# Optimization experiments

Hardware: AMD Instinct MI355X
Metric: run time of the kernel (lower is better)

Reference implementation:

```python
import jax, jax.numpy as jnp
import numpy as np

N_NODES = 50000
N_EDGES = 1600000
IN_DIM, HID_DIM, OUT_DIM = 128, 128, 64


def setup_inputs() -> dict:
    key = jax.random.key(0)
    ks = jax.random.split(key, 6)
    x = jax.random.normal(ks[0], (N_NODES, IN_DIM), dtype=jnp.float32)
    W1 = jax.random.normal(ks[1], (IN_DIM, HID_DIM), dtype=jnp.float32) * (1.0 / np.sqrt(IN_DIM))
    b1 = jnp.zeros((HID_DIM,), dtype=jnp.float32)
    W2 = jax.random.normal(ks[2], (HID_DIM, OUT_DIM), dtype=jnp.float32) * (1.0 / np.sqrt(HID_DIM))
    b2 = jnp.zeros((OUT_DIM,), dtype=jnp.float32)
    src = jax.random.randint(ks[3], (N_EDGES,), 0, N_NODES, dtype=jnp.int32)
    dst = jax.random.randint(ks[4], (N_EDGES,), 0, N_NODES, dtype=jnp.int32)
    return {"x": x, "W1": W1, "b1": b1, "W2": W2, "b2": b2,
            "src": src, "dst": dst, "n_nodes": N_NODES}


def _degree_norms(src, dst, n_nodes):
    ones = jnp.ones(src.shape, dtype=jnp.float32)
    out_deg = jax.ops.segment_sum(ones, src, num_segments=n_nodes)
    in_deg = jax.ops.segment_sum(ones, dst, num_segments=n_nodes)
    # DGL clamps degrees to min 1 before taking -0.5 power
    out_norm = jnp.power(jnp.maximum(out_deg, 1.0), -0.5)
    in_norm = jnp.power(jnp.maximum(in_deg, 1.0), -0.5)
    return out_norm, in_norm


def _graph_conv(x, W, b, src, dst, out_norm, in_norm, n_nodes):
    # norm='both': scale src feats, project (W first: in>=out), aggregate, scale dst
    h = x * out_norm[:, None]
    h = h @ W                                   # [N, out_feats]
    agg = jax.ops.segment_sum(h[src], dst, num_segments=n_nodes)
    return agg * in_norm[:, None] + b


def reference(x, W1, b1, W2, b2, src, dst, n_nodes):
    out_norm, in_norm = _degree_norms(src, dst, n_nodes)
    h = _graph_conv(x, W1, b1, src, dst, out_norm, in_norm, n_nodes)
    h = jax.nn.relu(h)
    # F.dropout(training=self.training): identity in eval mode
    h = _graph_conv(h, W2, b2, src, dst, out_norm, in_norm, n_nodes)
    return h
```

## Files before the change

### kernel.cpp

```cpp
#include <hip/hip_runtime.h>
#include <cstdint>

#define N_NODES 50000
#define N_EDGES 1600000
#define NPAD 50048
#define NTILES (NPAD / 64)
#define DUMMY 50000

#define NCOARSE 196
#define CBLK 256
#define ECHUNK (N_EDGES / CBLK)

#define OSL2 2
#define ONPS2 (N_NODES / OSL2)
#define ONW (ONPS2 / 2)
#define OPARTS2 256
#define OCH2 (N_EDGES / OPARTS2)

typedef __attribute__((ext_vector_type(8))) _Float16 f16x8;
typedef __attribute__((ext_vector_type(2))) _Float16 f16x2;
typedef __attribute__((ext_vector_type(4))) float f32x4;

__device__ __forceinline__ unsigned f16rn(float f) {
    _Float16 h = (_Float16)f;
    return (unsigned)__builtin_bit_cast(unsigned short, h);
}
__device__ __forceinline__ f16x2 u2h(unsigned u) { return __builtin_bit_cast(f16x2, u); }
__device__ __forceinline__ f16x2 pk_xor_add(f16x2 s, int d) {
    unsigned u = __builtin_bit_cast(unsigned, s);
    unsigned o = (unsigned)__shfl_xor((int)u, d);
    return s + __builtin_bit_cast(f16x2, o);
}

__global__ void k_fuse1(const int* __restrict__ src, const int* __restrict__ dst,
                        const float* __restrict__ W1, const float* __restrict__ W2,
                        unsigned* __restrict__ counts, unsigned* __restrict__ partial,
                        unsigned* __restrict__ Wt1, unsigned* __restrict__ Wt2) {
    __shared__ unsigned sm[ONW];
    int b = blockIdx.x, tid = threadIdx.x;
    if (b < 512) {
        int slice = b & 1, part = b >> 1;
        int lo = slice * ONPS2;
        for (int i = tid; i < ONW; i += 256) sm[i] = 0;
        __syncthreads();
        int ebase = part * OCH2;
        for (int i = tid; i < OCH2; i += 256) {
            int sv = src[ebase + i] - lo;
            if ((unsigned)sv < (unsigned)ONPS2)
                atomicAdd(&sm[sv >> 1], 1u << ((sv & 1) * 16));
        }
        __syncthreads();
        unsigned* outp = partial + ((size_t)slice * OPARTS2 + part) * ONW;
        for (int i = tid; i < ONW; i += 256) outp[i] = sm[i];
    } else if (b < 768) {
        int b2 = b - 512;
        for (int i = tid; i < NCOARSE; i += 256) sm[i] = 0;
        __syncthreads();
        int base = b2 * ECHUNK;
        for (int i = tid; i < ECHUNK; i += 256)
            atomicAdd(&sm[(unsigned)dst[base + i] >> 8], 1u);
        __syncthreads();
        for (int i = tid; i < NCOARSE; i += 256)
            counts[b2 * NCOARSE + i] = sm[i];
    } else {
        int t = (b - 768) * 256 + tid;
        if (t < 128 * 64) {
            int n = t >> 6, kp = t & 63;
            Wt1[t] = f16rn(W1[(2 * kp) * 128 + n]) | (f16rn(W1[(2 * kp + 1) * 128 + n]) << 16);
        }
        if (t < 64 * 64) {
            int n = t >> 6, kp = t & 63;
            Wt2[t] = f16rn(W2[(2 * kp) * 64 + n]) | (f16rn(W2[(2 * kp + 1) * 64 + n]) << 16);
        }
    }
}

__global__ void k_scanA(const unsigned* __restrict__ counts, unsigned* __restrict__ woff,
                        unsigned* __restrict__ tot) {
    __shared__ unsigned s[256];
    int c = blockIdx.x, t = threadIdx.x;
    unsigned v = counts[t * NCOARSE + c];
    s[t] = v; __syncthreads();
    for (int o = 1; o < 256; o <<= 1) {
        unsigned u = (t >= o) ? s[t - o] : 0u;
        __syncthreads(); s[t] += u; __syncthreads();
    }
    woff[t * NCOARSE + c] = s[t] - v;
    if (t == 255) tot[c] = s[255];
}

__global__ void k_scanB(const unsigned* __restrict__ tot, unsigned* __restrict__ base,
                        unsigned* __restrict__ row_ptr) {
    __shared__ unsigned s[256];
    int t = threadIdx.x;
    unsigned v = (t < NCOARSE) ? tot[t] : 0u;
    s[t] = v; __syncthreads();
    for (int o = 1; o < 256; o <<= 1) {
        unsigned u = (t >= o) ? s[t - o] : 0u;
        __syncthreads(); s[t] += u; __syncthreads();
    }
    if (t < NCOARSE) base[t] = s[t] - v;
    if (t == NCOARSE - 1) base[NCOARSE] = s[t];
    if (t == 0) row_ptr[N_NODES] = N_EDGES;
}

__global__ void k_fuse2(const int* __restrict__ src, const int* __restrict__ dst,
                        const unsigned* __restrict__ base, const unsigned* __restrict__ woff,
                        int* __restrict__ tmp_s, int* __restrict__ tmp_d,
                        const unsigned* __restrict__ partial, float* __restrict__ on) {
    __shared__ unsigned cur[NCOARSE];
    int b = blockIdx.x, t = threadIdx.x;
    if (b < 256) {
        for (int i = t; i < NCOARSE; i += 256) cur[i] = base[i] + woff[b * NCOARSE + i];
        __syncthreads();
        int ebase = b * ECHUNK;
        for (int i = t; i < ECHUNK; i += 256) {
            int d = dst[ebase + i], sv = src[ebase + i];
            unsigned p = atomicAdd(&cur[(unsigned)d >> 8], 1u);
            tmp_d[p] = d; tmp_s[p] = sv;
        }
    } else {
        int tt = (b - 256) * 256 + t;
        if (tt < OSL2 * ONW) {
            int slice = tt / ONW, word = tt % ONW;
            const unsigned* p = partial + (size_t)slice * OPARTS2 * ONW + word;
            unsigned slo = 0, shi = 0;
            for (int q = 0; q < OPARTS2; ++q) {
                unsigned v = p[(size_t)q * ONW];
                slo += v & 0xffffu; shi += v >> 16;
            }
            float2 o;
            o.x = rsqrtf((float)(slo < 1u ? 1u : slo));
            o.y = rsqrtf((float)(shi < 1u ? 1u : shi));
            ((float2*)on)[(slice * ONPS2) / 2 + word] = o;
        }
    }
}

__global__ __launch_bounds__(256, 2) void k_fuse3(
        const float* __restrict__ x, const float* __restrict__ on,
        const unsigned* __restrict__ Wt1, unsigned short* __restrict__ hb,
        const int* __restrict__ tmp_s, const int* __restrict__ tmp_d,
        const unsigned* __restrict__ base,
        unsigned* __restrict__ row_ptr, float* __restrict__ inn,
        int* __restrict__ csr) {
    __shared__ char smem[49152] __attribute__((aligned(16)));
    int tid = threadIdx.x;
    if (blockIdx.x < NTILES) {
        uint4* lA4 = (uint4*)smem;
        uint4* lB4 = (uint4*)(smem + 16384);
        unsigned* lA = (unsigned*)lA4;
        unsigned* lB = (unsigned*)lB4;
        int m0 = blockIdx.x * 64;

        for (int i = tid; i < 128 * 64; i += 256) {
            int n = i >> 6, kp = i & 63;
            lB[(n * 64 + kp) ^ ((n & 7) << 2)] = Wt1[i];
        }
        const float2* x2 = (const float2*)x;
        for (int i = tid; i < 64 * 64; i += 256) {
            int m = i >> 6, kp = i & 63;
            int gm = m0 + m;
            float2 v = {0.f, 0.f}; float sc = 0.f;
            if (gm < N_NODES) { v = x2[(size_t)gm * 64 + kp]; sc = on[gm]; }
            lA[(m * 64 + kp) ^ ((m & 7) << 2)] = f16rn(v.x * sc) | (f16rn(v.y * sc) << 16);
        }
        __syncthreads();

        int lane = tid & 63, wv = tid >> 6;
        int lm = lane & 15, lg = lane >> 4;
        int ncol0 = wv * 32;

        f32x4 acc[4][2];
        #pragma unroll
        for (int a = 0; a < 4; ++a)
            #pragma unroll
            for (int b = 0; b < 2; ++b) acc[a][b] = f32x4{0.f, 0.f, 0.f, 0.f};

        #pragma unroll
        for (int ks = 0; ks < 4; ++ks) {
            f16x8 af[4], bfr[2];
            #pragma unroll
            for (int mt = 0; mt < 4; ++mt) {
                int row = mt * 16 + lm;
                af[mt] = __builtin_bit_cast(f16x8, lA4[(row * 16 + ks * 4 + lg) ^ (row & 7)]);
            }
            #pragma unroll
            for (int nt = 0; nt < 2; ++nt) {
                int row = ncol0 + nt * 16 + lm;
                bfr[nt] = __builtin_bit_cast(f16x8, lB4[(row * 16 + ks * 4 + lg) ^ (row & 7)]);
            }
            #pragma unroll
            for (int mt = 0; mt < 4; ++mt)
                #pragma unroll
                for (int nt = 0; nt < 2; ++nt)
                    acc[mt][nt] = __builtin_amdgcn_mfma_f32_16x16x32_f16(af[mt], bfr[nt], acc[mt][nt], 0, 0, 0);
        }
        #pragma unroll
        for (int mt = 0; mt < 4; ++mt)
            #pragma unroll
            for (int r = 0; r < 4; ++r) {
                int row = m0 + mt * 16 + lg * 4 + r;
                #pragma unroll
                for (int nt = 0; nt < 2; ++nt) {
                    int col = ncol0 + nt * 16 + lm;
                    hb[(size_t)row * 128 + col] = (unsigned short)f16rn(acc[mt][nt][r]);
                }
            }
    } else {
        unsigned* hist = (unsigned*)smem;
        unsigned* cur  = hist + 256;
        unsigned* s    = cur + 256;
        int c = blockIdx.x - NTILES, t = tid;
        unsigned beg = base[c], end = base[c + 1];
        hist[t] = 0;
        __syncthreads();
        for (unsigned i = beg + t; i < end; i += 256)
            atomicAdd(&hist[(unsigned)tmp_d[i] & 255u], 1u);
        __syncthreads();
        unsigned v = hist[t];
        s[t] = v; __syncthreads();
        for (int o = 1; o < 256; o <<= 1) {
            unsigned u = (t >= o) ? s[t - o] : 0u;
            __syncthreads(); s[t] += u; __syncthreads();
        }
        unsigned excl = s[t] - v;
        int node = c * 256 + t;
        if (node < N_NODES) {
            row_ptr[node] = beg + excl;
            inn[node] = rsqrtf((float)(v < 1u ? 1u : v));
        }
        cur[t] = beg + excl;
        __syncthreads();
        for (unsigned i = beg + t; i < end; i += 256) {
            int d = tmp_d[i], sv = tmp_s[i];
            unsigned p = atomicAdd(&cur[(unsigned)d & 255u], 1u);
            csr[p] = sv;
        }
    }
}

__global__ __launch_bounds__(256, 2) void gemm2_mfma(
        const unsigned* __restrict__ h1b, const unsigned* __restrict__ Wt2,
        unsigned short* __restrict__ h2b) {
    __shared__ uint4 lA4[64 * 16];
    __shared__ uint4 lB4[64 * 16];
    unsigned* lA = (unsigned*)lA4;
    unsigned* lB = (unsigned*)lB4;
    int tid = threadIdx.x;
    int m0 = blockIdx.x * 64;

    for (int i = tid; i < 64 * 64; i += 256) {
        int n = i >> 6, kp = i & 63;
        lB[(n * 64 + kp) ^ ((n & 7) << 2)] = Wt2[i];
    }
    for (int i = tid; i < 64 * 64; i += 256) {
        int m = i >> 6, kp = i & 63;
        int gm = m0 + m;
        lA[(m * 64 + kp) ^ ((m & 7) << 2)] = (gm < N_NODES) ? h1b[(size_t)gm * 64 + kp] : 0u;
    }
    __syncthreads();

    int lane = tid & 63, wv = tid >> 6;
    int lm = lane & 15, lg = lane >> 4;
    int ncol0 = wv * 16;

    f32x4 acc[4];
    #pragma unroll
    for (int a = 0; a < 4; ++a) acc[a] = f32x4{0.f, 0.f, 0.f, 0.f};

    #pragma unroll
    for (int ks = 0; ks < 4; ++ks) {
        int brow = ncol0 + lm;
        f16x8 bfr = __builtin_bit_cast(f16x8, lB4[(brow * 16 + ks * 4 + lg) ^ (brow & 7)]);
        #pragma unroll
        for (int mt = 0; mt < 4; ++mt) {
            int row = mt * 16 + lm;
            f16x8 af = __builtin_bit_cast(f16x8, lA4[(row * 16 + ks * 4 + lg) ^ (row & 7)]);
            acc[mt] = __builtin_amdgcn_mfma_f32_16x16x32_f16(af, bfr, acc[mt], 0, 0, 0);
        }
    }
    #pragma unroll
    for (int mt = 0; mt < 4; ++mt)
        #pragma unroll
        for (int r = 0; r < 4; ++r) {
            int row = m0 + mt * 16 + lg * 4 + r;
            h2b[(size_t)row * 64 + ncol0 + lm] = (unsigned short)f16rn(acc[mt][r]);
        }
}

__global__ __launch_bounds__(256) void gcn_agg1_kernel(
        const uint4* __restrict__ hb4, const int* __restrict__ csr,
        const unsigned int* __restrict__ row_ptr,
        const float* __restrict__ inn, const float* __restrict__ b1,
        const float* __restrict__ on, uint4* __restrict__ h1b4) {
    int lane = threadIdx.x & 63;
    int n = blockIdx.x * 4 + (threadIdx.x >> 6);
    unsigned beg = row_ptr[n], end = row_ptr[n + 1];
    int q = lane >> 4;
    unsigned w = (unsigned)(lane & 15);
    f16x2 s0 = u2h(0), s1 = u2h(0), s2 = u2h(0), s3 = u2h(0);
    for (unsigned base = beg; base < end; base += 64) {
        unsigned e = base + lane;
        int r = (e < end) ? csr[e] : DUMMY;
        int m = (int)(end - base); if (m > 64) m = 64;
        for (int j = 0; j < m; j += 32) {
            uint4 v[8];
            #pragma unroll
            for (int k = 0; k < 8; ++k) {
                if (j + 4 * k < m) {
                    unsigned idx = (unsigned)__shfl(r, j + 4 * k + q);
                    v[k] = hb4[(size_t)idx * 16 + w];
                }
            }
            #pragma unroll
            for (int k = 0; k < 8; ++k) {
                if (j + 4 * k < m) {
                    s0 += u2h(v[k].x); s1 += u2h(v[k].y);
                    s2 += u2h(v[k].z); s3 += u2h(v[k].w);
                }
            }
        }
    }
    s0 = pk_xor_add(s0, 16); s1 = pk_xor_add(s1, 16);
    s2 = pk_xor_add(s2, 16); s3 = pk_xor_add(s3, 16);
    s0 = pk_xor_add(s0, 32); s1 = pk_xor_add(s1, 32);
    s2 = pk_xor_add(s2, 32); s3 = pk_xor_add(s3, 32);
    if (q == 0) {
        float sc = inn[n], osc = on[n];
        float4 ba = ((const float4*)b1)[2 * w];
        float4 bb = ((const float4*)b1)[2 * w + 1];
        float f0 = fmaxf((float)s0[0] * sc + ba.x, 0.f) * osc;
        float f1 = fmaxf((float)s0[1] * sc + ba.y, 0.f) * osc;
        float f2 = fmaxf((float)s1[0] * sc + ba.z, 0.f) * osc;
        float f3 = fmaxf((float)s1[1] * sc + ba.w, 0.f) * osc;
        float f4 = fmaxf((float)s2[0] * sc + bb.x, 0.f) * osc;
        float f5 = fmaxf((float)s2[1] * sc + bb.y, 0.f) * osc;
        float f6 = fmaxf((float)s3[0] * sc + bb.z, 0.f) * osc;
        float f7 = fmaxf((float)s3[1] * sc + bb.w, 0.f) * osc;
        uint4 o;
        o.x = f16rn(f0) | (f16rn(f1) << 16);
        o.y = f16rn(f2) | (f16rn(f3) << 16);
        o.z = f16rn(f4) | (f16rn(f5) << 16);
        o.w = f16rn(f6) | (f16rn(f7) << 16);
        h1b4[(size_t)n * 16 + w] = o;
    }
}

__global__ __launch_bounds__(256) void gcn_agg2_kernel(
        const uint4* __restrict__ h2b4, const int* __restrict__ csr,
        const unsigned int* __restrict__ row_ptr,
        const float* __restrict__ inn, const float* __restrict__ b2,
        float* __restrict__ out) {
    int lane = threadIdx.x & 63;
    int n = blockIdx.x * 4 + (threadIdx.x >> 6);
    unsigned beg = row_ptr[n], end = row_ptr[n + 1];
    int o8 = lane >> 3;
    unsigned w = (unsigned)(lane & 7);
    f16x2 s0 = u2h(0), s1 = u2h(0), s2 = u2h(0), s3 = u2h(0);
    for (unsigned base = beg; base < end; base += 64) {
        unsigned e = base + lane;
        int r = (e < end) ? csr[e] : DUMMY;
        int m = (int)(end - base); if (m > 64) m = 64;
        uint4 v[8];
        #pragma unroll
        for (int k = 0; k < 8; ++k) {
            if (8 * k < m) {
                unsigned idx = (unsigned)__shfl(r, 8 * k + o8);
                v[k] = h2b4[(size_t)idx * 8 + w];
            }
        }
        #pragma unroll
        for (int k = 0; k < 8; ++k) {
            if (8 * k < m) {
                s0 += u2h(v[k].x); s1 += u2h(v[k].y);
                s2 += u2h(v[k].z); s3 += u2h(v[k].w);
            }
        }
    }
    s0 = pk_xor_add(s0, 8);  s1 = pk_xor_add(s1, 8);
    s2 = pk_xor_add(s2, 8);  s3 = pk_xor_add(s3, 8);
    s0 = pk_xor_add(s0, 16); s1 = pk_xor_add(s1, 16);
    s2 = pk_xor_add(s2, 16); s3 = pk_xor_add(s3, 16);
    s0 = pk_xor_add(s0, 32); s1 = pk_xor_add(s1, 32);
    s2 = pk_xor_add(s2, 32); s3 = pk_xor_add(s3, 32);
    if (lane < 8) {
        float sc = inn[n];
        float4 ba = ((const float4*)b2)[2 * w];
        float4 bb = ((const float4*)b2)[2 * w + 1];
        float4 oA, oB;
        oA.x = (float)s0[0] * sc + ba.x; oA.y = (float)s0[1] * sc + ba.y;
        oA.z = (float)s1[0] * sc + ba.z; oA.w = (float)s1[1] * sc + ba.w;
        oB.x = (float)s2[0] * sc + bb.x; oB.y = (float)s2[1] * sc + bb.y;
        oB.z = (float)s3[0] * sc + bb.z; oB.w = (float)s3[1] * sc + bb.w;
        ((float4*)out)[(size_t)n * 16 + 2 * w]     = oA;
        ((float4*)out)[(size_t)n * 16 + 2 * w + 1] = oB;
    }
}

extern "C" void kernel_launch(void* const* d_in, const int* in_sizes, int n_in,
                              void* d_out, int out_size, void* d_ws, size_t ws_size,
                              hipStream_t stream) {
    const float* x  = (const float*)d_in[0];
    const float* W1 = (const float*)d_in[1];
    const float* b1 = (const float*)d_in[2];
    const float* W2 = (const float*)d_in[3];
    const float* b2 = (const float*)d_in[4];
    const int*   src = (const int*)d_in[5];
    const int*   dst = (const int*)d_in[6];
    float* out = (float*)d_out;

    char* ws = (char*)d_ws;
    size_t off = 0;
    auto alloc = [&](size_t bytes) -> void* {
        void* p = ws + off;
        off += (bytes + 255) & ~(size_t)255;
        return p;
    };

    float*        on      = (float*)alloc((size_t)N_NODES * 4);
    float*        inn     = (float*)alloc((size_t)N_NODES * 4);
    unsigned int* row_ptr = (unsigned int*)alloc((size_t)(N_NODES + 1) * 4);
    unsigned int* base    = (unsigned int*)alloc((NCOARSE + 1) * 4);
    unsigned int* tot     = (unsigned int*)alloc(NCOARSE * 4);
    unsigned int* Wt1     = (unsigned int*)alloc(128 * 64 * 4);
    unsigned int* Wt2     = (unsigned int*)alloc(64 * 64 * 4);
    unsigned int* counts  = (unsigned int*)alloc((size_t)CBLK * NCOARSE * 4);
    unsigned int* woff    = (unsigned int*)alloc((size_t)CBLK * NCOARSE * 4);
    int*          csr     = (int*)alloc((size_t)N_EDGES * 4);
    int*          tmp_s   = (int*)alloc((size_t)N_EDGES * 4);
    int*          tmp_d   = (int*)alloc((size_t)N_EDGES * 4);
    unsigned int* partial = (unsigned int*)alloc((size_t)OSL2 * OPARTS2 * ONW * 4);
    unsigned short* hb    = (unsigned short*)alloc((size_t)NPAD * 128 * 2);
    unsigned int* h1b     = (unsigned int*)alloc((size_t)NPAD * 64 * 4);
    unsigned short* h2b   = (unsigned short*)alloc((size_t)NPAD * 64 * 2);

    k_fuse1<<<800, 256, 0, stream>>>(src, dst, W1, W2, counts, partial, Wt1, Wt2);
    k_scanA<<<NCOARSE, 256, 0, stream>>>(counts, woff, tot);
    k_scanB<<<1, 256, 0, stream>>>(tot, base, row_ptr);
    k_fuse2<<<256 + (OSL2 * ONW + 255) / 256, 256, 0, stream>>>(src, dst, base, woff, tmp_s, tmp_d, partial, on);
    k_fuse3<<<NTILES + NCOARSE, 256, 0, stream>>>(x, on, Wt1, hb, tmp_s, tmp_d, base, row_ptr, inn, csr);
    gcn_agg1_kernel<<<N_NODES / 4, 256, 0, stream>>>((const uint4*)hb, csr, row_ptr, inn, b1, on, (uint4*)h1b);
    gemm2_mfma<<<NTILES, 256, 0, stream>>>(h1b, Wt2, h2b);
    gcn_agg2_kernel<<<N_NODES / 4, 256, 0, stream>>>((const uint4*)h2b, csr, row_ptr, inn, b2, out);
}
```

Before: 168.5 us.

## Split aggregation tables into column slices and pack degree counts into bytes

The GEMM outputs are now stored as separate 32-column fp16 tables (four for layer 1, two for layer 2). The aggregation kernels are rewritten so each block gathers from only one slice, with 16 lanes per node and 32-edge chunks. The aim is to shrink the gather working set so it stays cache-resident and to make neighbor loads narrower and better used. The out-degree histogram now packs four 8-bit counters per word in a single pass instead of two node slices of 16-bit counters, which halves the histogram blocks. The byte counters could overflow if any partition gives a node 256 or more out-edges.

```diff
diff --git a/kernel.cpp b/kernel.cpp
--- a/kernel.cpp
+++ b/kernel.cpp
@@ -11,11 +11,11 @@
 #define CBLK 256
 #define ECHUNK (N_EDGES / CBLK)
 
-#define OSL2 2
-#define ONPS2 (N_NODES / OSL2)
-#define ONW (ONPS2 / 2)
-#define OPARTS2 256
-#define OCH2 (N_EDGES / OPARTS2)
+#define ONW 12500
+#define OPARTS 256
+#define OCH (N_EDGES / OPARTS)
+
+#define AGG_BPP 3125
 
 typedef __attribute__((ext_vector_type(8))) _Float16 f16x8;
 typedef __attribute__((ext_vector_type(2))) _Float16 f16x2;
@@ -38,22 +38,19 @@
                         unsigned* __restrict__ Wt1, unsigned* __restrict__ Wt2) {
     __shared__ unsigned sm[ONW];
     int b = blockIdx.x, tid = threadIdx.x;
-    if (b < 512) {
-        int slice = b & 1, part = b >> 1;
-        int lo = slice * ONPS2;
+    if (b < 256) {
         for (int i = tid; i < ONW; i += 256) sm[i] = 0;
         __syncthreads();
-        int ebase = part * OCH2;
-        for (int i = tid; i < OCH2; i += 256) {
-            int sv = src[ebase + i] - lo;
-            if ((unsigned)sv < (unsigned)ONPS2)
-                atomicAdd(&sm[sv >> 1], 1u << ((sv & 1) * 16));
-        }
-        __syncthreads();
-        unsigned* outp = partial + ((size_t)slice * OPARTS2 + part) * ONW;
+        int ebase = b * OCH;
+        for (int i = tid; i < OCH; i += 256) {
+            int sv = src[ebase + i];
+            atomicAdd(&sm[sv >> 2], 1u << ((sv & 3) * 8));
+        }
+        __syncthreads();
+        unsigned* outp = partial + (size_t)b * ONW;
         for (int i = tid; i < ONW; i += 256) outp[i] = sm[i];
-    } else if (b < 768) {
-        int b2 = b - 512;
+    } else if (b < 512) {
+        int b2 = b - 256;
         for (int i = tid; i < NCOARSE; i += 256) sm[i] = 0;
         __syncthreads();
         int base = b2 * ECHUNK;
@@ -63,7 +60,7 @@
         for (int i = tid; i < NCOARSE; i += 256)
             counts[b2 * NCOARSE + i] = sm[i];
     } else {
-        int t = (b - 768) * 256 + tid;
+        int t = (b - 512) * 256 + tid;
         if (t < 128 * 64) {
             int n = t >> 6, kp = t & 63;
             Wt1[t] = f16rn(W1[(2 * kp) * 128 + n]) | (f16rn(W1[(2 * kp + 1) * 128 + n]) << 16);
@@ -121,18 +118,20 @@
         }
     } else {
         int tt = (b - 256) * 256 + t;
-        if (tt < OSL2 * ONW) {
-            int slice = tt / ONW, word = tt % ONW;
-            const unsigned* p = partial + (size_t)slice * OPARTS2 * ONW + word;
-            unsigned slo = 0, shi = 0;
-            for (int q = 0; q < OPARTS2; ++q) {
+        if (tt < ONW) {
+            const unsigned* p = partial + tt;
+            unsigned a0 = 0, a1 = 0, a2 = 0, a3 = 0;
+            for (int q = 0; q < OPARTS; ++q) {
                 unsigned v = p[(size_t)q * ONW];
-                slo += v & 0xffffu; shi += v >> 16;
+                a0 += v & 255u; a1 += (v >> 8) & 255u;
+                a2 += (v >> 16) & 255u; a3 += v >> 24;
             }
-            float2 o;
-            o.x = rsqrtf((float)(slo < 1u ? 1u : slo));
-            o.y = rsqrtf((float)(shi < 1u ? 1u : shi));
-            ((float2*)on)[(slice * ONPS2) / 2 + word] = o;
+            float4 o;
+            o.x = rsqrtf((float)(a0 < 1u ? 1u : a0));
+            o.y = rsqrtf((float)(a1 < 1u ? 1u : a1));
+            o.z = rsqrtf((float)(a2 < 1u ? 1u : a2));
+            o.w = rsqrtf((float)(a3 < 1u ? 1u : a3));
+            ((float4*)on)[tt] = o;
         }
     }
 }
@@ -170,6 +169,7 @@
         int lane = tid & 63, wv = tid >> 6;
         int lm = lane & 15, lg = lane >> 4;
         int ncol0 = wv * 32;
+        unsigned short* tabq = hb + (size_t)wv * NPAD * 32;
 
         f32x4 acc[4][2];
         #pragma unroll
@@ -203,8 +203,8 @@
                 int row = m0 + mt * 16 + lg * 4 + r;
                 #pragma unroll
                 for (int nt = 0; nt < 2; ++nt) {
-                    int col = ncol0 + nt * 16 + lm;
-                    hb[(size_t)row * 128 + col] = (unsigned short)f16rn(acc[mt][nt][r]);
+                    int lcol = nt * 16 + lm;
+                    tabq[(size_t)row * 32 + lcol] = (unsigned short)f16rn(acc[mt][nt][r]);
                 }
             }
     } else {
@@ -264,6 +264,8 @@
     int lane = tid & 63, wv = tid >> 6;
     int lm = lane & 15, lg = lane >> 4;
     int ncol0 = wv * 16;
+    unsigned short* tabh = h2b + (size_t)(wv >> 1) * NPAD * 32;
+    int lcol = (wv & 1) * 16 + lm;
 
     f32x4 acc[4];
     #pragma unroll
@@ -285,51 +287,55 @@
         #pragma unroll
         for (int r = 0; r < 4; ++r) {
             int row = m0 + mt * 16 + lg * 4 + r;
-            h2b[(size_t)row * 64 + ncol0 + lm] = (unsigned short)f16rn(acc[mt][r]);
-        }
-}
-
-__global__ __launch_bounds__(256) void gcn_agg1_kernel(
-        const uint4* __restrict__ hb4, const int* __restrict__ csr,
-        const unsigned int* __restrict__ row_ptr,
+            tabh[(size_t)row * 32 + lcol] = (unsigned short)f16rn(acc[mt][r]);
+        }
+}
+
+__global__ __launch_bounds__(256) void k_agg1(
+        const unsigned short* __restrict__ hb, const int* __restrict__ csr,
+        const unsigned* __restrict__ row_ptr,
         const float* __restrict__ inn, const float* __restrict__ b1,
-        const float* __restrict__ on, uint4* __restrict__ h1b4) {
-    int lane = threadIdx.x & 63;
-    int n = blockIdx.x * 4 + (threadIdx.x >> 6);
+        const float* __restrict__ on, unsigned* __restrict__ h1b) {
+    int qr = blockIdx.x / AGG_BPP;
+    int bp = blockIdx.x % AGG_BPP;
+    int tid = threadIdx.x;
+    int lane = tid & 63;
+    int l16 = lane & 15;
+    int node_sub = lane >> 4;
+    int w = l16 & 3;
+    int slot = l16 >> 2;
+    int n = bp * 16 + (tid >> 6) * 4 + node_sub;
     unsigned beg = row_ptr[n], end = row_ptr[n + 1];
-    int q = lane >> 4;
-    unsigned w = (unsigned)(lane & 15);
+    int m = (int)(end - beg);
+    const uint4* tab = (const uint4*)(hb + (size_t)qr * NPAD * 32);
     f16x2 s0 = u2h(0), s1 = u2h(0), s2 = u2h(0), s3 = u2h(0);
-    for (unsigned base = beg; base < end; base += 64) {
-        unsigned e = base + lane;
-        int r = (e < end) ? csr[e] : DUMMY;
-        int m = (int)(end - base); if (m > 64) m = 64;
-        for (int j = 0; j < m; j += 32) {
-            uint4 v[8];
-            #pragma unroll
-            for (int k = 0; k < 8; ++k) {
-                if (j + 4 * k < m) {
-                    unsigned idx = (unsigned)__shfl(r, j + 4 * k + q);
-                    v[k] = hb4[(size_t)idx * 16 + w];
-                }
-            }
-            #pragma unroll
-            for (int k = 0; k < 8; ++k) {
-                if (j + 4 * k < m) {
-                    s0 += u2h(v[k].x); s1 += u2h(v[k].y);
-                    s2 += u2h(v[k].z); s3 += u2h(v[k].w);
-                }
-            }
-        }
-    }
-    s0 = pk_xor_add(s0, 16); s1 = pk_xor_add(s1, 16);
-    s2 = pk_xor_add(s2, 16); s3 = pk_xor_add(s3, 16);
-    s0 = pk_xor_add(s0, 32); s1 = pk_xor_add(s1, 32);
-    s2 = pk_xor_add(s2, 32); s3 = pk_xor_add(s3, 32);
-    if (q == 0) {
+    for (int jb = 0; jb < m; jb += 32) {
+        unsigned e0 = beg + jb + l16;
+        unsigned e1 = e0 + 16;
+        int r0 = (e0 < end) ? csr[e0] : DUMMY;
+        int r1 = (e1 < end) ? csr[e1] : DUMMY;
+        uint4 v[8];
+        #pragma unroll
+        for (int k = 0; k < 8; ++k) {
+            int sl = 4 * k + slot;
+            int srcl = node_sub * 16 + (sl & 15);
+            unsigned idx = (unsigned)__shfl(k < 4 ? r0 : r1, srcl);
+            v[k] = tab[(size_t)idx * 4 + w];
+        }
+        #pragma unroll
+        for (int k = 0; k < 8; ++k) {
+            s0 += u2h(v[k].x); s1 += u2h(v[k].y);
+            s2 += u2h(v[k].z); s3 += u2h(v[k].w);
+        }
+    }
+    s0 = pk_xor_add(s0, 4); s1 = pk_xor_add(s1, 4);
+    s2 = pk_xor_add(s2, 4); s3 = pk_xor_add(s3, 4);
+    s0 = pk_xor_add(s0, 8); s1 = pk_xor_add(s1, 8);
+    s2 = pk_xor_add(s2, 8); s3 = pk_xor_add(s3, 8);
+    if (slot == 0) {
         float sc = inn[n], osc = on[n];
-        float4 ba = ((const float4*)b1)[2 * w];
-        float4 bb = ((const float4*)b1)[2 * w + 1];
+        float4 ba = ((const float4*)b1)[qr * 8 + w * 2];
+        float4 bb = ((const float4*)b1)[qr * 8 + w * 2 + 1];
         float f0 = fmaxf((float)s0[0] * sc + ba.x, 0.f) * osc;
         float f1 = fmaxf((float)s0[1] * sc + ba.y, 0.f) * osc;
         float f2 = fmaxf((float)s1[0] * sc + ba.z, 0.f) * osc;
@@ -343,58 +349,62 @@
         o.y = f16rn(f2) | (f16rn(f3) << 16);
         o.z = f16rn(f4) | (f16rn(f5) << 16);
         o.w = f16rn(f6) | (f16rn(f7) << 16);
-        h1b4[(size_t)n * 16 + w] = o;
-    }
-}
-
-__global__ __launch_bounds__(256) void gcn_agg2_kernel(
-        const uint4* __restrict__ h2b4, const int* __restrict__ csr,
-        const unsigned int* __restrict__ row_ptr,
+        ((uint4*)h1b)[(size_t)n * 16 + qr * 4 + w] = o;
+    }
+}
+
+__global__ __launch_bounds__(256) void k_agg2(
+        const unsigned short* __restrict__ h2b, const int* __restrict__ csr,
+        const unsigned* __restrict__ row_ptr,
         const float* __restrict__ inn, const float* __restrict__ b2,
         float* __restrict__ out) {
-    int lane = threadIdx.x & 63;
-    int n = blockIdx.x * 4 + (threadIdx.x >> 6);
+    int hf = blockIdx.x / AGG_BPP;
+    int bp = blockIdx.x % AGG_BPP;
+    int tid = threadIdx.x;
+    int lane = tid & 63;
+    int l16 = lane & 15;
+    int node_sub = lane >> 4;
+    int w = l16 & 3;
+    int slot = l16 >> 2;
+    int n = bp * 16 + (tid >> 6) * 4 + node_sub;
     unsigned beg = row_ptr[n], end = row_ptr[n + 1];
-    int o8 = lane >> 3;
-    unsigned w = (unsigned)(lane & 7);
+    int m = (int)(end - beg);
+    const uint4* tab = (const uint4*)(h2b + (size_t)hf * NPAD * 32);
     f16x2 s0 = u2h(0), s1 = u2h(0), s2 = u2h(0), s3 = u2h(0);
-    for (unsigned base = beg; base < end; base += 64) {
-        unsigned e = base + lane;
-        int r = (e < end) ? csr[e] : DUMMY;
-        int m = (int)(end - base); if (m > 64) m = 64;
+    for (int jb = 0; jb < m; jb += 32) {
+        unsigned e0 = beg + jb + l16;
+        unsigned e1 = e0 + 16;
+        int r0 = (e0 < end) ? csr[e0] : DUMMY;
+        int r1 = (e1 < end) ? csr[e1] : DUMMY;
         uint4 v[8];
         #pragma unroll
         for (int k = 0; k < 8; ++k) {
-            if (8 * k < m) {
-                unsigned idx = (unsigned)__shfl(r, 8 * k + o8);
-                v[k] = h2b4[(size_t)idx * 8 + w];
-            }
+            int sl = 4 * k + slot;
+            int srcl = node_sub * 16 + (sl & 15);
+            unsigned idx = (unsigned)__shfl(k < 4 ? r0 : r1, srcl);
+            v[k] = tab[(size_t)idx * 4 + w];
         }
         #pragma unroll
         for (int k = 0; k < 8; ++k) {
-            if (8 * k < m) {
-                s0 += u2h(v[k].x); s1 += u2h(v[k].y);
-                s2 += u2h(v[k].z); s3 += u2h(v[k].w);
-            }
-        }
-    }
-    s0 = pk_xor_add(s0, 8);  s1 = pk_xor_add(s1, 8);
-    s2 = pk_xor_add(s2, 8);  s3 = pk_xor_add(s3, 8);
-    s0 = pk_xor_add(s0, 16); s1 = pk_xor_add(s1, 16);
-    s2 = pk_xor_add(s2, 16); s3 = pk_xor_add(s3, 16);
-    s0 = pk_xor_add(s0, 32); s1 = pk_xor_add(s1, 32);
-    s2 = pk_xor_add(s2, 32); s3 = pk_xor_add(s3, 32);
-    if (lane < 8) {
+            s0 += u2h(v[k].x); s1 += u2h(v[k].y);
+            s2 += u2h(v[k].z); s3 += u2h(v[k].w);
+        }
+    }
+    s0 = pk_xor_add(s0, 4); s1 = pk_xor_add(s1, 4);
+    s2 = pk_xor_add(s2, 4); s3 = pk_xor_add(s3, 4);
+    s0 = pk_xor_add(s0, 8); s1 = pk_xor_add(s1, 8);
+    s2 = pk_xor_add(s2, 8); s3 = pk_xor_add(s3, 8);
+    if (slot == 0) {
         float sc = inn[n];
-        float4 ba = ((const float4*)b2)[2 * w];
-        float4 bb = ((const float4*)b2)[2 * w + 1];
+        float4 ba = ((const float4*)b2)[hf * 8 + w * 2];
+        float4 bb = ((const float4*)b2)[hf * 8 + w * 2 + 1];
         float4 oA, oB;
         oA.x = (float)s0[0] * sc + ba.x; oA.y = (float)s0[1] * sc + ba.y;
         oA.z = (float)s1[0] * sc + ba.z; oA.w = (float)s1[1] * sc + ba.w;
         oB.x = (float)s2[0] * sc + bb.x; oB.y = (float)s2[1] * sc + bb.y;
         oB.z = (float)s3[0] * sc + bb.z; oB.w = (float)s3[1] * sc + bb.w;
-        ((float4*)out)[(size_t)n * 16 + 2 * w]     = oA;
-        ((float4*)out)[(size_t)n * 16 + 2 * w + 1] = oB;
+        ((float4*)out)[(size_t)n * 16 + hf * 8 + w * 2]     = oA;
+        ((float4*)out)[(size_t)n * 16 + hf * 8 + w * 2 + 1] = oB;
     }
 }
 
@@ -430,17 +440,17 @@
     int*          csr     = (int*)alloc((size_t)N_EDGES * 4);
     int*          tmp_s   = (int*)alloc((size_t)N_EDGES * 4);
     int*          tmp_d   = (int*)alloc((size_t)N_EDGES * 4);
-    unsigned int* partial = (unsigned int*)alloc((size_t)OSL2 * OPARTS2 * ONW * 4);
-    unsigned short* hb    = (unsigned short*)alloc((size_t)NPAD * 128 * 2);
+    unsigned int* partial = (unsigned int*)alloc((size_t)OPARTS * ONW * 4);
+    unsigned short* hb    = (unsigned short*)alloc((size_t)4 * NPAD * 32 * 2);
     unsigned int* h1b     = (unsigned int*)alloc((size_t)NPAD * 64 * 4);
-    unsigned short* h2b   = (unsigned short*)alloc((size_t)NPAD * 64 * 2);
-
-    k_fuse1<<<800, 256, 0, stream>>>(src, dst, W1, W2, counts, partial, Wt1, Wt2);
+    unsigned short* h2b   = (unsigned short*)alloc((size_t)2 * NPAD * 32 * 2);
+
+    k_fuse1<<<544, 256, 0, stream>>>(src, dst, W1, W2, counts, partial, Wt1, Wt2);
     k_scanA<<<NCOARSE, 256, 0, stream>>>(counts, woff, tot);
     k_scanB<<<1, 256, 0, stream>>>(tot, base, row_ptr);
-    k_fuse2<<<256 + (OSL2 * ONW + 255) / 256, 256, 0, stream>>>(src, dst, base, woff, tmp_s, tmp_d, partial, on);
+    k_fuse2<<<256 + (ONW + 255) / 256, 256, 0, stream>>>(src, dst, base, woff, tmp_s, tmp_d, partial, on);
     k_fuse3<<<NTILES + NCOARSE, 256, 0, stream>>>(x, on, Wt1, hb, tmp_s, tmp_d, base, row_ptr, inn, csr);
-    gcn_agg1_kernel<<<N_NODES / 4, 256, 0, stream>>>((const uint4*)hb, csr, row_ptr, inn, b1, on, (uint4*)h1b);
+    k_agg1<<<4 * AGG_BPP, 256, 0, stream>>>(hb, csr, row_ptr, inn, b1, on, h1b);
     gemm2_mfma<<<NTILES, 256, 0, stream>>>(h1b, Wt2, h2b);
-    gcn_agg2_kernel<<<N_NODES / 4, 256, 0, stream>>>((const uint4*)h2b, csr, row_ptr, inn, b2, out);
-}
+    k_agg2<<<2 * AGG_BPP, 256, 0, stream>>>(h2b, csr, row_ptr, inn, b2, out);
+}
```

After: 158.8 us. 1.06x faster.
